# Kernel optimization log

Hardware: AMD Instinct MI355X
Metric: run time of the kernel (lower is better)

Reference implementation:

```python
import jax, jax.numpy as jnp
import numpy as np
import math

B, L, IN, HID, H, NL = 2, 1024, 512, 1024, 16, 2
DH = HID // H


def _rel_shift(x):
    # Transformer-XL relative shift for the position-bias term (the pos_lookup).
    # x: [B, H, L, P] with P == L; out[b,h,i,j] uses relative distance (i - j).
    b, h, l, p = x.shape
    x = jnp.pad(x, ((0, 0), (0, 0), (0, 0), (1, 0)))
    return x.reshape(b, h, p + 1, l)[:, :, 1:, :].reshape(b, h, l, p)


def _ln(v, w, bias, eps=1e-12):
    # BertLayerNorm: epsilon inside the sqrt
    u = v.mean(-1, keepdims=True)
    s = ((v - u) ** 2).mean(-1, keepdims=True)
    return w * (v - u) / jnp.sqrt(s + eps) + bias


def _gelu(v):
    # exact erf-based GELU as in the source
    return v * 0.5 * (1.0 + jax.lax.erf(v / math.sqrt(2.0)))


def _forward(x, pos_raw, Wh1, bh1, Wh2, bh2, Wq, bq, Wk, bk, Wv, bv, Wp, bp,
             cbias, pbias, Wo, bo, Wf1, bf1, Wf2, bf2, ln_w, ln_b):
    # to_hidden MLP: input_size -> hidden -> hidden with GELU
    h = _gelu(x @ Wh1 + bh1) @ Wh2 + bh2  # [B, L, HID]
    scale = 1.0 / math.sqrt(DH)
    for l in range(Wq.shape[0]):
        # per-head LinearSplit projections, fused into one einsum per Q/K/V/pos
        q = jnp.einsum('bld,hdk->blhk', h, Wq[l]) + bq[l]
        k = jnp.einsum('bld,hdk->blhk', h, Wk[l]) + bk[l]
        v = jnp.einsum('bld,hdk->blhk', h, Wv[l]) + bv[l]
        p = jnp.einsum('pd,hdk->hpk', pos_raw, Wp[l]) + bp[l][:, None, :]
        qc = q + cbias[l]  # content-biased query
        qp = q + pbias[l]  # position-biased query
        ac = jnp.einsum('bihk,bjhk->bhij', qc, k)                 # content score
        bd = _rel_shift(jnp.einsum('bihk,hpk->bhip', qp, p))      # position score
        w = jax.nn.softmax((ac + bd) * scale, axis=-1)            # [B,H,L,L]
        a = jnp.einsum('bhij,bjhk->bihk', w, v)
        a = a.reshape(h.shape[0], h.shape[1], -1)                 # combine heads
        a = a @ Wo[l] + bo[l]
        h1 = _ln(a + h, ln_w[l], ln_b[l])                         # residual + LN
        f = _gelu(h1 @ Wf1[l] + bf1[l]) @ Wf2[l] + bf2[l]         # top FFN
        h = _ln(h1 + f, ln_w[l], ln_b[l])                         # shared LN params
    return h


def setup_inputs() -> dict:
    key = jax.random.key(0)
    ks = iter(jax.random.split(key, 32))
    n = lambda shape, s=0.02: jax.random.normal(next(ks), shape, dtype=jnp.float32) * s
    return {
        'x': jax.random.normal(next(ks), (B, L, IN), dtype=jnp.float32),
        'pos_raw': jax.random.normal(next(ks), (L, HID), dtype=jnp.float32),
        'Wh1': n((IN, HID)), 'bh1': jnp.zeros((HID,), jnp.float32),
        'Wh2': n((HID, HID)), 'bh2': jnp.zeros((HID,), jnp.float32),
        'Wq': n((NL, H, HID, DH)), 'bq': jnp.zeros((NL, H, DH), jnp.float32),
        'Wk': n((NL, H, HID, DH)), 'bk': jnp.zeros((NL, H, DH), jnp.float32),
        'Wv': n((NL, H, HID, DH)), 'bv': jnp.zeros((NL, H, DH), jnp.float32),
        'Wp': n((NL, H, HID, DH)), 'bp': jnp.zeros((NL, H, DH), jnp.float32),
        'cbias': n((NL, H, DH), 1.0), 'pbias': n((NL, H, DH), 1.0),
        'Wo': n((NL, HID, HID)), 'bo': jnp.zeros((NL, HID), jnp.float32),
        'Wf1': n((NL, HID, HID)), 'bf1': jnp.zeros((NL, HID), jnp.float32),
        'Wf2': n((NL, HID, HID)), 'bf2': jnp.zeros((NL, HID), jnp.float32),
        'ln_w': jnp.ones((NL, HID), jnp.float32),
        'ln_b': jnp.zeros((NL, HID), jnp.float32),
    }


def reference(x, pos_raw, Wh1, bh1, Wh2, bh2, Wq, bq, Wk, bk, Wv, bv, Wp, bp,
              cbias, pbias, Wo, bo, Wf1, bf1, Wf2, bf2, ln_w, ln_b):
    return _forward(x, pos_raw, Wh1, bh1, Wh2, bh2, Wq, bq, Wk, bk, Wv, bv,
                    Wp, bp, cbias, pbias, Wo, bo, Wf1, bf1, Wf2, bf2, ln_w, ln_b)
```

## Files before the change

### kernel.cpp

```cpp
#include <hip/hip_runtime.h>
#include <hip/hip_bf16.h>
#include <math.h>

typedef unsigned short u16;
typedef __attribute__((ext_vector_type(8))) short bhalf8;
typedef __attribute__((ext_vector_type(4))) float f32x4;

#define DEV __device__ __forceinline__

DEV float bf2f(u16 u){ unsigned int i=((unsigned int)u)<<16; float f; __builtin_memcpy(&f,&i,4); return f; }
DEV u16 f2bf(float f){ unsigned int i; __builtin_memcpy(&i,&f,4); i += 0x7FFFu + ((i>>16)&1u); return (u16)(i>>16); }
DEV float gelu_f(float x){ return 0.5f*x*(1.0f+erff(x*0.70710678118654752f)); }
DEV float wredsum(float v){ for(int o=32;o;o>>=1) v+=__shfl_down(v,o); return v; }

DEV void gload16(const u16* g, u16* l){
  __builtin_amdgcn_global_load_lds(
      (const __attribute__((address_space(1))) void*)g,
      (__attribute__((address_space(3))) void*)l, 16, 0, 0);
}

#define KAPPA 0.18033688011112042f
#define ZSTR 1049664L

template<int BM, int BN, int EPI>
__global__ __launch_bounds__(256, 2) void gemm_bt(
    const u16* __restrict__ A, const u16* __restrict__ Bt,
    void* __restrict__ C0, void* __restrict__ C1, void* __restrict__ C2,
    const float* __restrict__ bias0, const float* __restrict__ bias1,
    int M, int N, int K, int lda, int ldb, int ldc, int Hdiv, int bst,
    long sAb, long sAh, long sBb, long sBh, long sCb, long sCh)
{
  constexpr int FM = BM/32, FN = BN/32;
  constexpr int NL = (BM+BN)/32;
  static_assert(NL==6 || NL==4, "vmcnt literal for this tile not wired");
  __shared__ __align__(16) u16 sA[2][BM][64];
  __shared__ __align__(16) u16 sB[2][BN][64];
  const int bflat = blockIdx.y * gridDim.x + blockIdx.x;
  const int bq = bflat >> 3, br = bflat & 7;
  int bx, by;
  if (gridDim.x == 48){
    by = 8*(br & 1) + (bq & 7);
    bx = 12*(br >> 1) + (bq >> 3);
  } else {
    const int kb = (gridDim.y==32) ? 2 : (gridDim.y==16) ? 1 : 0;
    by = br + 8*(bq & ((1<<kb)-1));
    bx = bq >> kb;
  }
  const int z  = blockIdx.z;
  const int bb = z / Hdiv, hh = z % Hdiv;
  const u16* Ab = A + (long)bb*sAb + (long)hh*sAh + (long)by*BM*lda;
  const u16* Bb = Bt + (long)bb*sBb + (long)hh*sBh + (long)bx*BN*ldb;
  const long coff = (long)bb*sCb + (long)hh*sCh;
  const int m0 = by*BM, n0 = bx*BN;
  const int tid = threadIdx.x, lane = tid&63, wave = tid>>6;
  const int wm = wave>>1, wn = wave&1;
  const int rl = lane&15, g = lane>>4;
  const int rswz = rl & 7;

  auto stage = [&](int buf, int kt){
    #pragma unroll
    for (int i=0;i<BM/32;i++){
      int idx = i*256 + tid;
      int r = idx>>3, s = (idx&7) ^ (r&7);
      gload16(Ab + (long)r*lda + kt + s*8, &sA[buf][0][0] + (long)(i*256 + wave*64)*8);
    }
    #pragma unroll
    for (int i=0;i<BN/32;i++){
      int idx = i*256 + tid;
      int r = idx>>3, s = (idx&7) ^ (r&7);
      gload16(Bb + (long)r*ldb + kt + s*8, &sB[buf][0][0] + (long)(i*256 + wave*64)*8);
    }
  };

  f32x4 acc[FM][FN] = {};
  const int nt = K >> 6;
  stage(0, 0);
  int cur = 0;
  for (int t=0; t<nt; ++t){
    if (t+1 < nt){
      stage(cur^1, (t+1)<<6);
      if constexpr (NL==6) asm volatile("s_waitcnt vmcnt(6)" ::: "memory");
      else                 asm volatile("s_waitcnt vmcnt(4)" ::: "memory");
    } else {
      asm volatile("s_waitcnt vmcnt(0)" ::: "memory");
    }
    __builtin_amdgcn_s_barrier();
    #pragma unroll
    for (int ks=0; ks<2; ++ks){
      bhalf8 af[FM], bfr[FN];
      #pragma unroll
      for (int i=0;i<FM;i++){
        int row = wm*(BM/2)+i*16+rl;
        af[i]  = *(const bhalf8*)&sA[cur][row][(((ks*4+g)) ^ rswz)*8];
      }
      #pragma unroll
      for (int j=0;j<FN;j++){
        int row = wn*(BN/2)+j*16+rl;
        bfr[j] = *(const bhalf8*)&sB[cur][row][(((ks*4+g)) ^ rswz)*8];
      }
      #pragma unroll
      for (int i=0;i<FM;i++)
        #pragma unroll
        for (int j=0;j<FN;j++)
          acc[i][j] = __builtin_amdgcn_mfma_f32_16x16x32_bf16(af[i], bfr[j], acc[i][j], 0,0,0);
    }
    __builtin_amdgcn_s_barrier();
    cur ^= 1;
  }
  const int cr = g*4, cc = rl;
  #pragma unroll
  for (int i=0;i<FM;i++){
    const int gm = m0 + wm*(BM/2) + i*16 + cr;
    #pragma unroll
    for (int j=0;j<FN;j++){
      const int gn = n0 + wn*(BN/2) + j*16 + cc;
      const float b0v = (EPI&(1|64)) ? bias0[(long)bb*bst + gn] : 0.0f;
      const float b1v = (EPI&8) ? bias1[gn] : 0.0f;
      f32x4 v = acc[i][j];
      if (EPI&64){
        if (gn >= 2048){
          ushort4 w4 = { f2bf(v[0]+b0v), f2bf(v[1]+b0v), f2bf(v[2]+b0v), f2bf(v[3]+b0v) };
          const long vbase = ((long)(gm>>10))*1048576L + (long)(gn-2048)*1024 + (gm&1023);
          *(ushort4*)((u16*)C2 + vbase) = w4;
        } else {
          #pragma unroll
          for (int jj=0;jj<4;jj++){
            ((u16*)C0)[(long)(gm+jj)*ldc + gn] = f2bf(v[jj] + b0v);
            if (gn < 1024)
              ((u16*)C1)[(long)(gm+jj)*1024 + gn] = f2bf(v[jj] + bias1[gn]);
          }
        }
        continue;
      }
      #pragma unroll
      for (int jj=0;jj<4;jj++){
        const long cidx = coff + (long)(gm+jj)*ldc + gn;
        float o0 = v[jj] + b0v;
        if (EPI&2)  o0 = gelu_f(o0);
        if (EPI&4)  ((u16*)C0)[cidx] = f2bf(o0);
        else        ((float*)C0)[cidx] = o0;
        if (EPI&8)  ((u16*)C1)[cidx] = f2bf(v[jj] + b1v);
        if (EPI&16) ((float*)C1)[cidx] = o0;
      }
    }
  }
}

template<int BM, int BN, int EPI>
static void launch_gemm(hipStream_t s, int M,int N,int K,
    const u16* A,int lda,long sAb,long sAh,
    const u16* Bt,int ldb,long sBb,long sBh,
    void* C0, void* C1, void* C2, int ldc, long sCb, long sCh,
    const float* b0, const float* b1, int bst, int NB, int HD)
{
  gemm_bt<BM,BN,EPI><<<dim3(N/BN, M/BM, NB), dim3(256), 0, s>>>(
      A,Bt,C0,C1,C2,b0,b1,M,N,K,lda,ldb,ldc,HD,bst,sAb,sAh,sBb,sBh,sCb,sCh);
}

__global__ __launch_bounds__(256) void flash_attn(
    const u16* __restrict__ qkv,
    const u16* __restrict__ vtb,
    const u16* __restrict__ bdf,
    u16* __restrict__ ab)
{
  const int z = blockIdx.y, b = z >> 4, h = z & 15;
  const int i0 = blockIdx.x * 64;
  const int tid = threadIdx.x, lane = tid & 63, wave = tid >> 6;
  const int rl = lane & 15, g = lane >> 4;
  const int ig = i0 + wave*16 + rl;

  __shared__ u16 kt[128][68];
  __shared__ u16 vt[64][132];
  __shared__ u16 pw[4][16][132];

  const u16* qrow = qkv + ((long)(b*1024 + ig))*3072 + h*64;
  const bhalf8 qf0 = *(const bhalf8*)(qrow + g*8);
  const bhalf8 qf1 = *(const bhalf8*)(qrow + 32 + g*8);
  const u16* bdbase = bdf + (long)z*ZSTR + 1 + ((long)ig<<10) + 1023 + g*4;

  bhalf8 kreg[2][2], vreg[2][2];
  ushort4 bdreg[2][8];

  auto issueKV = [&](int jt){
    #pragma unroll
    for (int w = 0; w < 2; ++w){
      int r = (tid>>2) + w*64, c = tid&3;
      const u16* sk = qkv + ((long)(b*1024 + jt*128 + r))*3072 + 1024 + h*64 + c*16;
      kreg[w][0] = *(const bhalf8*)(sk);
      kreg[w][1] = *(const bhalf8*)(sk + 8);
      int d = (tid>>3) + w*32, c2 = tid&7;
      const u16* sv = vtb + (long)b*1048576L + ((long)(h*64 + d))*1024 + jt*128 + c2*16;
      vreg[w][0] = *(const bhalf8*)(sv);
      vreg[w][1] = *(const bhalf8*)(sv + 8);
    }
  };

  issueKV(0);
  {
    #pragma unroll
    for (int jf = 0; jf < 8; ++jf) bdreg[0][jf] = *(const ushort4*)(bdbase + jf*16);
  }

  f32x4 o[4] = {};
  float m = -INFINITY, l = 0.f;

  #pragma unroll
  for (int jt = 0; jt < 8; ++jt){
    __syncthreads();
    #pragma unroll
    for (int w = 0; w < 2; ++w){
      int r = (tid>>2) + w*64, c = tid&3;
      *(bhalf8*)&kt[r][c*16]     = kreg[w][0];
      *(bhalf8*)&kt[r][c*16 + 8] = kreg[w][1];
      int d = (tid>>3) + w*32, c2 = tid&7;
      *(bhalf8*)&vt[d][c2*16]     = vreg[w][0];
      *(bhalf8*)&vt[d][c2*16 + 8] = vreg[w][1];
    }
    __syncthreads();

    if (jt < 7){
      issueKV(jt+1);
      const u16* p = bdbase + (jt+1)*128;
      #pragma unroll
      for (int jf = 0; jf < 8; ++jf) bdreg[(jt+1)&1][jf] = *(const ushort4*)(p + jf*16);
    }

    f32x4 s[8];
    __builtin_amdgcn_s_setprio(1);
    #pragma unroll
    for (int jf = 0; jf < 8; ++jf){
      bhalf8 a0 = *(const bhalf8*)&kt[jf*16 + rl][g*8];
      bhalf8 a1 = *(const bhalf8*)&kt[jf*16 + rl][32 + g*8];
      f32x4 acc = {};
      acc = __builtin_amdgcn_mfma_f32_16x16x32_bf16(a0, qf0, acc, 0,0,0);
      acc = __builtin_amdgcn_mfma_f32_16x16x32_bf16(a1, qf1, acc, 0,0,0);
      ushort4 bdv = bdreg[jt&1][jf];
      acc[0] += bf2f(bdv.x); acc[1] += bf2f(bdv.y);
      acc[2] += bf2f(bdv.z); acc[3] += bf2f(bdv.w);
      s[jf] = acc;
    }
    __builtin_amdgcn_s_setprio(0);

    float mt = s[0][0];
    #pragma unroll
    for (int jf = 0; jf < 8; ++jf)
      #pragma unroll
      for (int r2 = 0; r2 < 4; ++r2) mt = fmaxf(mt, s[jf][r2]);
    mt = fmaxf(mt, __shfl_xor(mt, 16));
    mt = fmaxf(mt, __shfl_xor(mt, 32));
    if (__any(mt > m + 11.5f)){
      const float mnew = fmaxf(m, mt);
      const float alpha = exp2f(m - mnew);
      l *= alpha;
      #pragma unroll
      for (int df = 0; df < 4; ++df) o[df] *= alpha;
      m = mnew;
    }
    float psum = 0.f;
    #pragma unroll
    for (int jf = 0; jf < 8; ++jf)
      #pragma unroll
      for (int r2 = 0; r2 < 4; ++r2){
        float p = exp2f(s[jf][r2] - m);
        psum += p; s[jf][r2] = p;
      }
    psum += __shfl_xor(psum, 16);
    psum += __shfl_xor(psum, 32);
    l += psum;

    #pragma unroll
    for (int jf = 0; jf < 8; ++jf){
      uint2 pk;
      pk.x = (unsigned)f2bf(s[jf][0]) | ((unsigned)f2bf(s[jf][1])<<16);
      pk.y = (unsigned)f2bf(s[jf][2]) | ((unsigned)f2bf(s[jf][3])<<16);
      *(uint2*)&pw[wave][rl][jf*16 + g*4] = pk;
    }

    __builtin_amdgcn_s_setprio(1);
    #pragma unroll
    for (int df = 0; df < 4; ++df)
      #pragma unroll
      for (int kf = 0; kf < 4; ++kf){
        bhalf8 a  = *(const bhalf8*)&vt[df*16 + rl][kf*32 + g*8];
        bhalf8 bf = *(const bhalf8*)&pw[wave][rl][kf*32 + g*8];
        o[df] = __builtin_amdgcn_mfma_f32_16x16x32_bf16(a, bf, o[df], 0,0,0);
      }
    __builtin_amdgcn_s_setprio(0);
  }

  const float rlv = 1.0f / l;
  u16* orow = ab + ((long)(b*1024 + ig))*1024 + h*64;
  #pragma unroll
  for (int df = 0; df < 4; ++df){
    ushort4 w4;
    w4.x = f2bf(o[df][0]*rlv); w4.y = f2bf(o[df][1]*rlv);
    w4.z = f2bf(o[df][2]*rlv); w4.w = f2bf(o[df][3]*rlv);
    *(ushort4*)(orow + df*16 + g*4) = w4;
  }
}

__global__ __launch_bounds__(256) void ln_kernel(
    const float* __restrict__ xa, const float* __restrict__ xb2,
    const float* __restrict__ gamma, const float* __restrict__ beta,
    u16* __restrict__ ob, float* __restrict__ of)
{
  const long row = blockIdx.x;
  const int tid = threadIdx.x;
  const float4 a4 = ((const float4*)(xa  + row*1024))[tid];
  const float4 b4 = ((const float4*)(xb2 + row*1024))[tid];
  float v[4] = {a4.x+b4.x, a4.y+b4.y, a4.z+b4.z, a4.w+b4.w};
  float s = v[0]+v[1]+v[2]+v[3];
  __shared__ float red[4];
  s = wredsum(s);
  const int lane = tid&63, w = tid>>6;
  if (!lane) red[w] = s;
  __syncthreads();
  const float mean = (red[0]+red[1]+red[2]+red[3]) * (1.0f/1024.0f);
  float q = 0.f;
  #pragma unroll
  for (int k=0;k<4;k++){ float d = v[k]-mean; q += d*d; }
  __syncthreads();
  q = wredsum(q);
  if (!lane) red[w] = q;
  __syncthreads();
  const float var = (red[0]+red[1]+red[2]+red[3]) * (1.0f/1024.0f);
  const float rstd = rsqrtf(var + 1e-12f);
  const float4 g4 = ((const float4*)gamma)[tid];
  const float4 be4 = ((const float4*)beta)[tid];
  float oo[4];
  oo[0] = g4.x*(v[0]-mean)*rstd + be4.x;
  oo[1] = g4.y*(v[1]-mean)*rstd + be4.y;
  oo[2] = g4.z*(v[2]-mean)*rstd + be4.z;
  oo[3] = g4.w*(v[3]-mean)*rstd + be4.w;
  ushort4 ob4 = { f2bf(oo[0]), f2bf(oo[1]), f2bf(oo[2]), f2bf(oo[3]) };
  *(ushort4*)(ob + row*1024 + tid*4) = ob4;
  float4 of4 = { oo[0], oo[1], oo[2], oo[3] };
  ((float4*)(of + row*1024))[tid] = of4;
}

struct TJobs {
  const float* src[16];
  u16* dst[16];
  int R[16], C[16], nb[16];
  float sc[16];
};

__global__ __launch_bounds__(256) void wprep(TJobs J)
{
  const int j = blockIdx.y;
  const int R = J.R[j], C = J.C[j];
  const float scl = J.sc[j];
  const int tR = R>>5, tC = C>>5;
  const int ntiles = tR*tC*J.nb[j];
  const int t = blockIdx.x;
  if (t >= ntiles) return;
  const int b = t/(tR*tC); const int t2 = t%(tR*tC);
  const int tr = t2/tC, tc = t2%tC;
  const float* src = J.src[j] + (long)b*R*C;
  u16* dst = J.dst[j] + (long)b*R*C;
  __shared__ float tl[32][33];
  const int tx = threadIdx.x & 31, ty = threadIdx.x >> 5;
  #pragma unroll
  for (int k=0;k<4;k++){ int r = ty + k*8; tl[r][tx] = src[(long)(tr*32+r)*C + tc*32 + tx]; }
  __syncthreads();
  #pragma unroll
  for (int k=0;k<4;k++){ int r = ty + k*8;
    dst[(long)(tc*32 + r)*R + tr*32 + tx] = f2bf(tl[tx][r]*scl); }
}

__global__ __launch_bounds__(256) void misc_prep(
    const float* __restrict__ x, const float* __restrict__ pos,
    const float* __restrict__ bq, const float* __restrict__ cb, const float* __restrict__ pbv,
    const float* __restrict__ bk, const float* __restrict__ bv,
    u16* __restrict__ xb, u16* __restrict__ posb,
    float* __restrict__ bqkv, float* __restrict__ bqp,
    u16* __restrict__ bd)
{
  const int n1 = 2048*512, n2 = 1024*1024, n3 = 8192;
  int idx = blockIdx.x*256 + threadIdx.x;
  if (idx < n1) { xb[idx] = f2bf(x[idx]); return; }
  idx -= n1;
  if (idx < n2) { posb[idx] = f2bf(pos[idx]); return; }
  idx -= n2;
  if (idx < n3) {
    int l = idx >> 12; int r = idx & 4095;
    if (r < 3072){
      float val;
      if (r < 1024)       val = (bq[l*1024+r] + cb[l*1024+r]) * KAPPA;
      else if (r < 2048)  val = bk[l*1024 + r-1024];
      else                val = bv[l*1024 + r-2048];
      bqkv[l*3072+r] = val;
    } else {
      int n = r - 3072;
      bqp[l*1024+n] = (bq[l*1024+n] + pbv[l*1024+n]) * KAPPA;
    }
    return;
  }
  idx -= n3;
  if (idx < 32*1024) {
    int z = idx >> 10, i = idx & 1023;
    bd[(long)z*ZSTR + 1 + (long)i*1025 + 1024] = 0;
  }
}

extern "C" void kernel_launch(void* const* d_in, const int* in_sizes, int n_in,
                              void* d_out, int out_size, void* d_ws, size_t ws_size,
                              hipStream_t stream)
{
  (void)in_sizes; (void)n_in; (void)out_size; (void)ws_size;
  const float* x    = (const float*)d_in[0];
  const float* pos  = (const float*)d_in[1];
  const float* Wh1  = (const float*)d_in[2];
  const float* bh1  = (const float*)d_in[3];
  const float* Wh2  = (const float*)d_in[4];
  const float* bh2  = (const float*)d_in[5];
  const float* Wq   = (const float*)d_in[6];
  const float* bq   = (const float*)d_in[7];
  const float* Wk   = (const float*)d_in[8];
  const float* bk   = (const float*)d_in[9];
  const float* Wv   = (const float*)d_in[10];
  const float* bv   = (const float*)d_in[11];
  const float* Wp   = (const float*)d_in[12];
  const float* bp   = (const float*)d_in[13];
  const float* cbias= (const float*)d_in[14];
  const float* pbias= (const float*)d_in[15];
  const float* Wo   = (const float*)d_in[16];
  const float* bo   = (const float*)d_in[17];
  const float* Wf1  = (const float*)d_in[18];
  const float* bf1  = (const float*)d_in[19];
  const float* Wf2  = (const float*)d_in[20];
  const float* bf2  = (const float*)d_in[21];
  const float* lnw  = (const float*)d_in[22];
  const float* lnb  = (const float*)d_in[23];

  const long EL = 1048576L;
  char* ws = (char*)d_ws;
  size_t off = 0;
  auto alloc = [&](size_t bytes)->char* {
    char* p = ws + off; off += (bytes + 255) & ~(size_t)255; return p;
  };
  u16* xb    = (u16*)alloc(2048L*512*2);
  u16* posb  = (u16*)alloc(EL*2);
  u16* Wh1t  = (u16*)alloc(512L*1024*2);
  u16* Wh2t  = (u16*)alloc(EL*2);
  u16* Wqkvt = (u16*)alloc(6*EL*2);
  u16* Wpt   = (u16*)alloc(2*EL*2);
  u16* Wot   = (u16*)alloc(2*EL*2);
  u16* Wf1t  = (u16*)alloc(2*EL*2);
  u16* Wf2t  = (u16*)alloc(2*EL*2);
  float* bqkv= (float*)alloc(2*3072*4);
  float* bqp = (float*)alloc(2*1024*4);
  u16* t1    = (u16*)alloc(2048L*1024*2);
  u16* hb    = (u16*)alloc(2048L*1024*2);
  float* hf  = (float*)alloc(2048L*1024*4);
  u16* qkvb  = (u16*)alloc(2048L*3072*2);
  u16* qp    = (u16*)alloc(2048L*1024*2);
  u16* vtb   = (u16*)alloc(2048L*1024*2);
  u16* pb    = (u16*)alloc(2*EL*2);
  u16* bd    = (u16*)alloc(32L*ZSTR*2);
  u16* ab    = (u16*)alloc(2048L*1024*2);
  float* aof = (float*)alloc(2048L*1024*4);
  u16* h1b   = (u16*)alloc(2048L*1024*2);
  float* h1f = (float*)alloc(2048L*1024*4);
  u16* f1b   = (u16*)alloc(2048L*1024*2);
  float* f2f = (float*)alloc(2048L*1024*4);

  misc_prep<<<dim3((2048*512 + 1024*1024 + 8192 + 32*1024 + 255)/256),
              dim3(256), 0, stream>>>(
      x, pos, bq, cbias, pbias, bk, bv, xb, posb, bqkv, bqp, bd);

  TJobs J; int ji = 0;
  auto addjob = [&](const float* s, u16* d, int R, int C, int nb, float sc){
    J.src[ji]=s; J.dst[ji]=d; J.R[ji]=R; J.C[ji]=C; J.nb[ji]=nb; J.sc[ji]=sc; ji++;
  };
  addjob(Wh1, Wh1t, 512, 1024, 1, 1.f);
  addjob(Wh2, Wh2t, 1024, 1024, 1, 1.f);
  for (int l=0;l<2;l++) addjob(Wq + l*EL, Wqkvt + l*3*EL,        1024, 64, 16, KAPPA);
  for (int l=0;l<2;l++) addjob(Wk + l*EL, Wqkvt + l*3*EL + EL,   1024, 64, 16, 1.f);
  for (int l=0;l<2;l++) addjob(Wv + l*EL, Wqkvt + l*3*EL + 2*EL, 1024, 64, 16, 1.f);
  for (int l=0;l<2;l++) addjob(Wp + l*EL, Wpt + l*EL, 1024, 64, 16, 1.f);
  for (int l=0;l<2;l++) addjob(Wo + l*EL, Wot + l*EL, 1024, 1024, 1, 1.f);
  for (int l=0;l<2;l++) addjob(Wf1 + l*EL, Wf1t + l*EL, 1024, 1024, 1, 1.f);
  for (int l=0;l<2;l++) addjob(Wf2 + l*EL, Wf2t + l*EL, 1024, 1024, 1, 1.f);
  wprep<<<dim3(1024, 16), dim3(256), 0, stream>>>(J);

  launch_gemm<64,64,7>(stream, 2048,1024,512,  xb,512,0,0,  Wh1t,512,0,0,
                 t1,nullptr,nullptr,1024,0,0,  bh1,nullptr, 0, 1,1);
  launch_gemm<64,64,21>(stream, 2048,1024,1024, t1,1024,0,0, Wh2t,1024,0,0,
                 hb,hf,nullptr,1024,0,0,  bh2,nullptr, 0, 1,1);

  launch_gemm<64,64,5>(stream, 1024,1024,1024, posb,1024, 0,0, Wpt,1024, EL,0,
                 pb,nullptr,nullptr,1024, EL,0,  bp,nullptr, 1024, 2,1);

  for (int l=0; l<2; l++){
    const u16 *Wqkvt_l = Wqkvt + l*3*EL, *Wot_l = Wot + l*EL,
              *Wf1t_l = Wf1t + l*EL, *Wf2t_l = Wf2t + l*EL;
    launch_gemm<128,64,64>(stream, 2048,3072,1024, hb,1024,0,0, Wqkvt_l,1024,0,0,
                    qkvb,qp,vtb,3072,0,0,  bqkv + l*3072, bqp + l*1024, 0, 1,1);
    launch_gemm<128,64,4>(stream, 1024,1024,64,  qp,1024, EL,64,  pb + l*EL,1024, 0,64,
                    bd+1,nullptr,nullptr,1025, 16L*ZSTR, ZSTR,  nullptr,nullptr, 0, 32,16);
    flash_attn<<<dim3(16,32), dim3(256), 0, stream>>>(qkvb, vtb, bd, ab);
    launch_gemm<64,64,1>(stream, 2048,1024,1024, ab,1024,0,0, Wot_l,1024,0,0,
                    aof,nullptr,nullptr,1024,0,0,  bo + l*1024, nullptr, 0, 1,1);
    ln_kernel<<<dim3(2048), dim3(256), 0, stream>>>(aof, hf, lnw + l*1024, lnb + l*1024, h1b, h1f);
    launch_gemm<64,64,7>(stream, 2048,1024,1024, h1b,1024,0,0, Wf1t_l,1024,0,0,
                    f1b,nullptr,nullptr,1024,0,0,  bf1 + l*1024, nullptr, 0, 1,1);
    launch_gemm<64,64,1>(stream, 2048,1024,1024, f1b,1024,0,0, Wf2t_l,1024,0,0,
                    f2f,nullptr,nullptr,1024,0,0,  bf2 + l*1024, nullptr, 0, 1,1);
    float* outf = (l==1) ? (float*)d_out : hf;
    ln_kernel<<<dim3(2048), dim3(256), 0, stream>>>(f2f, h1f, lnw + l*1024, lnb + l*1024, hb, outf);
  }
}
```

Baseline: 320.0 us.

## Split attention over key dimension into two halves with a combine kernel

The flash attention kernel now splits the 1024 keys into two halves along a third grid dimension, doubling the block count from 512 to 1024. Each half writes unnormalized fp32 partial outputs plus its running max and sum, and a new combine kernel merges them with log-sum-exp weights into the bf16 attention output. This aims to fill the many compute units on MI355X better, since the original grid was small. The cost is extra fp32 partial-output traffic (about 16 MB per layer) and one more kernel launch per layer.

```diff
diff --git a/kernel.cpp b/kernel.cpp
--- a/kernel.cpp
+++ b/kernel.cpp
@@ -161,9 +161,12 @@
     const u16* __restrict__ qkv,
     const u16* __restrict__ vtb,
     const u16* __restrict__ bdf,
-    u16* __restrict__ ab)
+    float* __restrict__ Opart,
+    float2* __restrict__ stats)
 {
   const int z = blockIdx.y, b = z >> 4, h = z & 15;
+  const int jh = blockIdx.z;
+  const int jt0 = jh * 4;
   const int i0 = blockIdx.x * 64;
   const int tid = threadIdx.x, lane = tid & 63, wave = tid >> 6;
   const int rl = lane & 15, g = lane >> 4;
@@ -195,17 +198,19 @@
     }
   };
 
-  issueKV(0);
+  issueKV(jt0);
   {
-    #pragma unroll
-    for (int jf = 0; jf < 8; ++jf) bdreg[0][jf] = *(const ushort4*)(bdbase + jf*16);
+    const u16* p = bdbase + jt0*128;
+    #pragma unroll
+    for (int jf = 0; jf < 8; ++jf) bdreg[0][jf] = *(const ushort4*)(p + jf*16);
   }
 
   f32x4 o[4] = {};
   float m = -INFINITY, l = 0.f;
 
   #pragma unroll
-  for (int jt = 0; jt < 8; ++jt){
+  for (int t = 0; t < 4; ++t){
+    const int jt = jt0 + t;
     __syncthreads();
     #pragma unroll
     for (int w = 0; w < 2; ++w){
@@ -218,11 +223,11 @@
     }
     __syncthreads();
 
-    if (jt < 7){
+    if (t < 3){
       issueKV(jt+1);
       const u16* p = bdbase + (jt+1)*128;
       #pragma unroll
-      for (int jf = 0; jf < 8; ++jf) bdreg[(jt+1)&1][jf] = *(const ushort4*)(p + jf*16);
+      for (int jf = 0; jf < 8; ++jf) bdreg[(t+1)&1][jf] = *(const ushort4*)(p + jf*16);
     }
 
     f32x4 s[8];
@@ -234,7 +239,7 @@
       f32x4 acc = {};
       acc = __builtin_amdgcn_mfma_f32_16x16x32_bf16(a0, qf0, acc, 0,0,0);
       acc = __builtin_amdgcn_mfma_f32_16x16x32_bf16(a1, qf1, acc, 0,0,0);
-      ushort4 bdv = bdreg[jt&1][jf];
+      ushort4 bdv = bdreg[t&1][jf];
       acc[0] += bf2f(bdv.x); acc[1] += bf2f(bdv.y);
       acc[2] += bf2f(bdv.z); acc[3] += bf2f(bdv.w);
       s[jf] = acc;
@@ -288,14 +293,40 @@
     __builtin_amdgcn_s_setprio(0);
   }
 
-  const float rlv = 1.0f / l;
-  u16* orow = ab + ((long)(b*1024 + ig))*1024 + h*64;
-  #pragma unroll
-  for (int df = 0; df < 4; ++df){
+  float* op = Opart + (((long)jh*32 + z)*1024 + ig)*64 + g*4;
+  #pragma unroll
+  for (int df = 0; df < 4; ++df)
+    *(f32x4*)(op + df*16) = o[df];
+  if (g == 0)
+    stats[((long)jh*32 + z)*1024 + ig] = make_float2(m, l);
+}
+
+__global__ __launch_bounds__(256) void attn_combine(
+    const float* __restrict__ Op, const float2* __restrict__ st,
+    u16* __restrict__ ab)
+{
+  const int z = blockIdx.y, b = z >> 4, h = z & 15;
+  const int i = blockIdx.x*64 + (threadIdx.x >> 2);
+  const int dg = threadIdx.x & 3;
+  const long r1 = ((long)z*1024 + i)*64 + dg*16;
+  const long r2 = r1 + 2097152L;
+  const float2 s1 = st[(long)z*1024 + i];
+  const float2 s2 = st[32L*1024 + (long)z*1024 + i];
+  const float M = fmaxf(s1.x, s2.x);
+  float w1 = exp2f(s1.x - M), w2 = exp2f(s2.x - M);
+  const float inv = 1.0f/(w1*s1.y + w2*s2.y);
+  w1 *= inv; w2 *= inv;
+  u16* orow = ab + ((long)(b*1024 + i))*1024 + h*64 + dg*16;
+  #pragma unroll
+  for (int k=0;k<4;k++){
+    f32x4 o1 = *(const f32x4*)(Op + r1 + k*4);
+    f32x4 o2 = *(const f32x4*)(Op + r2 + k*4);
     ushort4 w4;
-    w4.x = f2bf(o[df][0]*rlv); w4.y = f2bf(o[df][1]*rlv);
-    w4.z = f2bf(o[df][2]*rlv); w4.w = f2bf(o[df][3]*rlv);
-    *(ushort4*)(orow + df*16 + g*4) = w4;
+    w4.x = f2bf(w1*o1[0] + w2*o2[0]);
+    w4.y = f2bf(w1*o1[1] + w2*o2[1]);
+    w4.z = f2bf(w1*o1[2] + w2*o2[2]);
+    w4.w = f2bf(w1*o1[3] + w2*o2[3]);
+    *(ushort4*)(orow + k*4) = w4;
   }
 }
 
@@ -458,6 +489,8 @@
   u16* vtb   = (u16*)alloc(2048L*1024*2);
   u16* pb    = (u16*)alloc(2*EL*2);
   u16* bd    = (u16*)alloc(32L*ZSTR*2);
+  float* Opart = (float*)alloc(2L*32*1024*64*4);
+  float2* stats = (float2*)alloc(2L*32*1024*8);
   u16* ab    = (u16*)alloc(2048L*1024*2);
   float* aof = (float*)alloc(2048L*1024*4);
   u16* h1b   = (u16*)alloc(2048L*1024*2);
@@ -499,7 +532,8 @@
                     qkvb,qp,vtb,3072,0,0,  bqkv + l*3072, bqp + l*1024, 0, 1,1);
     launch_gemm<128,64,4>(stream, 1024,1024,64,  qp,1024, EL,64,  pb + l*EL,1024, 0,64,
                     bd+1,nullptr,nullptr,1025, 16L*ZSTR, ZSTR,  nullptr,nullptr, 0, 32,16);
-    flash_attn<<<dim3(16,32), dim3(256), 0, stream>>>(qkvb, vtb, bd, ab);
+    flash_attn<<<dim3(16,32,2), dim3(256), 0, stream>>>(qkvb, vtb, bd, Opart, stats);
+    attn_combine<<<dim3(16,32), dim3(256), 0, stream>>>(Opart, stats, ab);
     launch_gemm<64,64,1>(stream, 2048,1024,1024, ab,1024,0,0, Wot_l,1024,0,0,
                     aof,nullptr,nullptr,1024,0,0,  bo + l*1024, nullptr, 0, 1,1);
     ln_kernel<<<dim3(2048), dim3(256), 0, stream>>>(aof, hf, lnw + l*1024, lnb + l*1024, h1b, h1f);
```

Result: slower. 336.9 us (+5.3%).
